# Kernel optimization log

Measured on AMD Instinct MI355X. Metric: run time of the kernel, lower is better.

The kernel has to match this reference:

```python
import jax, jax.numpy as jnp
import numpy as np

N_NODES = 100000
N_EDGES = 800000
F_IN, HID, N_CLS = 256, 128, 32


def setup_inputs() -> dict:
    key = jax.random.key(0)
    k1, k2, k3, k4, k5 = jax.random.split(key, 5)
    features = jax.random.normal(k1, (N_NODES, F_IN), dtype=jnp.float32)
    # random directed edges with no self loops (so add_remaining_self_loops == append all loops)
    src = jax.random.randint(k2, (N_EDGES,), 0, N_NODES)
    off = jax.random.randint(k3, (N_EDGES,), 1, N_NODES)
    dst = (src + off) % N_NODES
    edge_index = jnp.stack([src, dst]).astype(jnp.int64)
    # Glorot-style params for the two GCNConv layers
    W1 = jax.random.normal(k4, (F_IN, HID), dtype=jnp.float32) * (1.0 / np.sqrt(F_IN))
    b1 = jnp.zeros((HID,), dtype=jnp.float32)
    W2 = jax.random.normal(k5, (HID, N_CLS), dtype=jnp.float32) * (1.0 / np.sqrt(HID))
    b2 = jnp.zeros((N_CLS,), dtype=jnp.float32)
    return {"features": features, "edge_index": edge_index, "W1": W1, "b1": b1, "W2": W2, "b2": b2}


def _gcn_conv(x, W, b, src, dst, norm, n):
    xw = x @ W                                  # [N, d_out] dense GEMM
    msg = xw[src] * norm[:, None]               # gather + scale, [E, d_out]
    out = jax.ops.segment_sum(msg, dst, num_segments=n)  # scatter-add to targets
    return out + b


def reference(features, edge_index, W1, b1, W2, b2):
    n = features.shape[0]
    # add_remaining_self_loops (input has none, so append all)
    loops = jnp.arange(n, dtype=edge_index.dtype)
    src = jnp.concatenate([edge_index[0], loops])
    dst = jnp.concatenate([edge_index[1], loops])
    # gcn_norm: deg over targets, sym normalization deg^-1/2 A deg^-1/2
    deg = jax.ops.segment_sum(jnp.ones_like(src, dtype=features.dtype), dst, num_segments=n)
    dinv = jnp.where(deg > 0, jax.lax.rsqrt(deg), 0.0)
    norm = dinv[src] * dinv[dst]
    x = _gcn_conv(features, W1, b1, src, dst, norm, n)
    x = jax.nn.relu(x)
    # dropout is identity at inference (training=False)
    x = _gcn_conv(x, W2, b2, src, dst, norm, n)
    return jax.nn.log_softmax(x, axis=1)
```

## Files before the change

kernel.cpp:

```cpp
#include <hip/hip_runtime.h>
#include <hip/hip_bf16.h>

typedef __bf16 bf16_t;
typedef __attribute__((ext_vector_type(8))) __bf16 bf16x8;
typedef __attribute__((ext_vector_type(4))) float f32x4;

__global__ void k_deg_count(const int* __restrict__ dst, int* __restrict__ deg, int E) {
    int e = blockIdx.x * blockDim.x + threadIdx.x;
    if (e < E) atomicAdd(&deg[dst[e]], 1);
}

__global__ __launch_bounds__(256) void k_dinv_scan1(const int* __restrict__ deg,
                                                    float* __restrict__ dinv,
                                                    int* __restrict__ bsum, int n) {
    __shared__ int red[256];
    int b = blockIdx.x, t = threadIdx.x;
    int base = b * 1024 + t * 4;
    int s = 0;
#pragma unroll
    for (int j = 0; j < 4; ++j) {
        int i = base + j;
        if (i < n) { int d = deg[i]; s += d; dinv[i] = rsqrtf((float)(d + 1)); }
    }
    red[t] = s;
    __syncthreads();
    for (int d = 128; d > 0; d >>= 1) {
        if (t < d) red[t] += red[t + d];
        __syncthreads();
    }
    if (t == 0) bsum[b] = red[0];
}

__global__ __launch_bounds__(256) void k_scan2(int* __restrict__ bsum, int nb,
                                               int* __restrict__ rowPtr, int n) {
    __shared__ int s[256];
    int t = threadIdx.x;
    int v = (t < nb) ? bsum[t] : 0;
    s[t] = v;
    __syncthreads();
    for (int d = 1; d < 256; d <<= 1) {
        int u = (t >= d) ? s[t - d] : 0;
        __syncthreads();
        s[t] += u;
        __syncthreads();
    }
    if (t < nb) bsum[t] = s[t] - v;
    if (t == 255) rowPtr[n] = s[255];
}

__global__ __launch_bounds__(256) void k_scan3(const int* __restrict__ deg,
                                               const int* __restrict__ bsum,
                                               int* __restrict__ rowPtr, int n) {
    __shared__ int red[256];
    int b = blockIdx.x, t = threadIdx.x;
    int base = b * 1024 + t * 4;
    int v[4]; int s = 0;
#pragma unroll
    for (int j = 0; j < 4; ++j) { int i = base + j; v[j] = (i < n) ? deg[i] : 0; s += v[j]; }
    red[t] = s;
    __syncthreads();
    for (int d = 1; d < 256; d <<= 1) {
        int u = (t >= d) ? red[t - d] : 0;
        __syncthreads();
        red[t] += u;
        __syncthreads();
    }
    int run = bsum[b] + red[t] - s;
#pragma unroll
    for (int j = 0; j < 4; ++j) { int i = base + j; if (i < n) rowPtr[i] = run; run += v[j]; }
}

__global__ void k_scatter(const int* __restrict__ src, const int* __restrict__ dst,
                          const float* __restrict__ dinv, const int* __restrict__ rowPtr,
                          int* __restrict__ cursor, int2* __restrict__ edata, int E) {
    int e = blockIdx.x * blockDim.x + threadIdx.x;
    if (e >= E) return;
    int s = src[e], d = dst[e];
    int pos = rowPtr[d] + atomicAdd(&cursor[d], 1);
    int2 p; p.x = s; p.y = __float_as_int(dinv[s] * dinv[d]);
    edata[pos] = p;
}

__device__ inline void packB_one(const float* __restrict__ B, bf16_t* __restrict__ Bp,
                                 int N, int idx) {
    int j    = idx & 7;
    int lane = (idx >> 3) & 63;
    int st   = idx >> 9;
    int nt   = N >> 4;
    int s = st / nt, t = st - s * nt;
    int k = s * 32 + (lane >> 4) * 8 + j;
    int n = t * 16 + (lane & 15);
    Bp[idx] = (bf16_t)B[(size_t)k * N + n];
}

__global__ void k_packBoth(const float* __restrict__ W1, bf16_t* __restrict__ Bp1,
                           const float* __restrict__ W2, bf16_t* __restrict__ Bp2) {
    int idx = blockIdx.x * blockDim.x + threadIdx.x;
    const int T1 = (256 / 32) * (128 / 16) * 512;
    const int T2 = (128 / 32) * (32 / 16) * 512;
    if (idx < T1) packB_one(W1, Bp1, 128, idx);
    else if (idx < T1 + T2) packB_one(W2, Bp2, 32, idx - T1);
}

template <int KSTEPS, int NTILES>
__global__ __launch_bounds__(256) void k_gemm_pf32(
        const float* __restrict__ A, const bf16_t* __restrict__ Bp,
        bf16_t* __restrict__ C, int M) {
    int wave = (blockIdx.x * blockDim.x + threadIdx.x) >> 6;
    if (wave * 16 >= M) return;
    int lane = threadIdx.x & 63;
    int r16 = lane & 15, quad = lane >> 4;
    const int K = KSTEPS * 32, N = NTILES * 16;
    f32x4 acc[NTILES] = {};
    const float* arow = A + (size_t)(wave * 16 + r16) * K + quad * 8;
#pragma unroll
    for (int s = 0; s < KSTEPS; ++s) {
        const float* ap = arow + s * 32;
        bf16x8 a;
#pragma unroll
        for (int j = 0; j < 8; ++j) a[j] = (bf16_t)ap[j];
        const bf16_t* bp = Bp + ((size_t)(s * NTILES) * 64 + lane) * 8;
#pragma unroll
        for (int t = 0; t < NTILES; ++t) {
            bf16x8 b = *(const bf16x8*)(bp + t * 512);
            acc[t] = __builtin_amdgcn_mfma_f32_16x16x32_bf16(a, b, acc[t], 0, 0, 0);
        }
    }
#pragma unroll
    for (int t = 0; t < NTILES; ++t)
#pragma unroll
        for (int r = 0; r < 4; ++r)
            C[(size_t)(wave * 16 + quad * 4 + r) * N + t * 16 + r16] = (bf16_t)acc[t][r];
}

template <int KSTEPS, int NTILES>
__global__ __launch_bounds__(256) void k_gemm_pa16(
        const bf16_t* __restrict__ A, const bf16_t* __restrict__ Bp,
        bf16_t* __restrict__ C, int M) {
    int wave = (blockIdx.x * blockDim.x + threadIdx.x) >> 6;
    if (wave * 16 >= M) return;
    int lane = threadIdx.x & 63;
    int r16 = lane & 15, quad = lane >> 4;
    const int K = KSTEPS * 32, N = NTILES * 16;
    f32x4 acc[NTILES] = {};
    const bf16_t* arow = A + (size_t)(wave * 16 + r16) * K + quad * 8;
#pragma unroll
    for (int s = 0; s < KSTEPS; ++s) {
        bf16x8 a = *(const bf16x8*)(arow + s * 32);
        const bf16_t* bp = Bp + ((size_t)(s * NTILES) * 64 + lane) * 8;
#pragma unroll
        for (int t = 0; t < NTILES; ++t) {
            bf16x8 b = *(const bf16x8*)(bp + t * 512);
            acc[t] = __builtin_amdgcn_mfma_f32_16x16x32_bf16(a, b, acc[t], 0, 0, 0);
        }
    }
#pragma unroll
    for (int t = 0; t < NTILES; ++t)
#pragma unroll
        for (int r = 0; r < 4; ++r)
            C[(size_t)(wave * 16 + quad * 4 + r) * N + t * 16 + r16] = (bf16_t)acc[t][r];
}

__global__ __launch_bounds__(256) void k_agg1(
        const int* __restrict__ rowPtr, const int2* __restrict__ edata,
        const bf16_t* __restrict__ XW1, const float* __restrict__ dinv,
        const float* __restrict__ b1, bf16_t* __restrict__ H, int n) {
    int wave = (blockIdx.x * blockDim.x + threadIdx.x) >> 6;
    if (wave >= n) return;
    int lane = threadIdx.x & 63;
    int fl = (lane & 15) << 3;
    int h  = lane >> 4;
    int r0 = rowPtr[wave], r1 = rowPtr[wave + 1];
    float a0[8] = {}, a1[8] = {};
    int k = r0 + h;
    for (; k + 4 < r1; k += 8) {
        int2 e0 = edata[k], e1 = edata[k + 4];
        float w0 = __int_as_float(e0.y), w1 = __int_as_float(e1.y);
        bf16x8 x0 = *(const bf16x8*)(XW1 + ((size_t)e0.x << 7) + fl);
        bf16x8 x1 = *(const bf16x8*)(XW1 + ((size_t)e1.x << 7) + fl);
#pragma unroll
        for (int j = 0; j < 8; ++j) { a0[j] += (float)x0[j] * w0; a1[j] += (float)x1[j] * w1; }
    }
    if (k < r1) {
        int2 e0 = edata[k];
        float w0 = __int_as_float(e0.y);
        bf16x8 x0 = *(const bf16x8*)(XW1 + ((size_t)e0.x << 7) + fl);
#pragma unroll
        for (int j = 0; j < 8; ++j) a0[j] += (float)x0[j] * w0;
    }
#pragma unroll
    for (int j = 0; j < 8; ++j) {
        a0[j] += a1[j];
        a0[j] += __shfl_xor(a0[j], 16);
        a0[j] += __shfl_xor(a0[j], 32);
    }
    if (h == 0) {
        float d = dinv[wave], d2 = d * d;
        bf16x8 xs = *(const bf16x8*)(XW1 + ((size_t)wave << 7) + fl);
        bf16x8 hv;
#pragma unroll
        for (int j = 0; j < 8; ++j) {
            float v = a0[j] + (float)xs[j] * d2 + b1[fl + j];
            hv[j] = (bf16_t)fmaxf(v, 0.f);
        }
        *(bf16x8*)(H + ((size_t)wave << 7) + fl) = hv;
    }
}

__global__ __launch_bounds__(256) void k_agg2(
        const int* __restrict__ rowPtr, const int2* __restrict__ edata,
        const bf16_t* __restrict__ XW2, const float* __restrict__ dinv,
        const float* __restrict__ b2, float* __restrict__ out, int n) {
    int wave = (blockIdx.x * blockDim.x + threadIdx.x) >> 6;
    if (wave >= n) return;
    int lane = threadIdx.x & 63;
    int f = lane & 31, h = lane >> 5;
    int r0 = rowPtr[wave], r1 = rowPtr[wave + 1];
    float acc0 = 0.f, acc1 = 0.f;
    int k = r0 + h;
    for (; k + 2 < r1; k += 4) {
        int2 e0 = edata[k], e1 = edata[k + 2];
        acc0 += (float)XW2[((size_t)e0.x << 5) + f] * __int_as_float(e0.y);
        acc1 += (float)XW2[((size_t)e1.x << 5) + f] * __int_as_float(e1.y);
    }
    if (k < r1) {
        int2 e0 = edata[k];
        acc0 += (float)XW2[((size_t)e0.x << 5) + f] * __int_as_float(e0.y);
    }
    float acc = acc0 + acc1;
    acc += __shfl_xor(acc, 32);
    float d = dinv[wave];
    float v = acc + (float)XW2[((size_t)wave << 5) + f] * d * d + b2[f];
    float mx = v;
#pragma unroll
    for (int m = 16; m >= 1; m >>= 1) mx = fmaxf(mx, __shfl_xor(mx, m));
    float s = expf(v - mx);
#pragma unroll
    for (int m = 16; m >= 1; m >>= 1) s += __shfl_xor(s, m);
    if (lane < 32) out[((size_t)wave << 5) + f] = v - mx - logf(s);
}

extern "C" void kernel_launch(void* const* d_in, const int* in_sizes, int n_in,
                              void* d_out, int out_size, void* d_ws, size_t ws_size,
                              hipStream_t stream) {
    const float* feat = (const float*)d_in[0];
    const int*   eidx = (const int*)d_in[1];
    const float* W1   = (const float*)d_in[2];
    const float* b1   = (const float*)d_in[3];
    const float* W2   = (const float*)d_in[4];
    const float* b2   = (const float*)d_in[5];
    float* out = (float*)d_out;

    const int FIN = 256, HID = 128, NCLS = 32;
    const int N = in_sizes[0] / FIN;
    const int E = in_sizes[1] / 2;
    const int* src = eidx;
    const int* dst = eidx + E;

    char* ws = (char*)d_ws;
    size_t o = 0;
    auto alloc = [&](size_t bytes) -> void* {
        void* p = ws + o;
        o = (o + bytes + 255) & ~(size_t)255;
        return p;
    };
    int*    deg    = (int*)   alloc((size_t)N * 4);
    int*    cursor = (int*)   alloc((size_t)N * 4);
    size_t  zlen   = (size_t)((char*)(cursor + N) - (char*)deg);
    float*  dinv   = (float*) alloc((size_t)N * 4);
    int*    rowPtr = (int*)   alloc((size_t)(N + 1) * 4);
    int*    bsum   = (int*)   alloc(256 * 4);
    bf16_t* Bp1    = (bf16_t*)alloc((size_t)(FIN / 32) * (HID / 16) * 512 * 2);
    bf16_t* Bp2    = (bf16_t*)alloc((size_t)(HID / 32) * (NCLS / 16) * 512 * 2);
    int2*   edata  = (int2*)  alloc((size_t)E * 8);
    bf16_t* XW1    = (bf16_t*)alloc((size_t)N * HID * 2);
    bf16_t* H      = (bf16_t*)alloc((size_t)N * HID * 2);
    bf16_t* XW2    = XW1;

    const int T = 256;
    const int NB = (N + 1023) >> 10;
    hipMemsetAsync(deg, 0, zlen, stream);
    k_deg_count <<<(E + T - 1) / T, T, 0, stream>>>(dst, deg, E);
    k_dinv_scan1<<<NB, T, 0, stream>>>(deg, dinv, bsum, N);
    k_scan2     <<<1, T, 0, stream>>>(bsum, NB, rowPtr, N);
    k_scan3     <<<NB, T, 0, stream>>>(deg, bsum, rowPtr, N);
    k_scatter   <<<(E + T - 1) / T, T, 0, stream>>>(src, dst, dinv, rowPtr, cursor, edata, E);
    k_packBoth  <<<(32768 + 4096 + T - 1) / T, T, 0, stream>>>(W1, Bp1, W2, Bp2);

    {
        int waves = (N + 15) / 16;
        k_gemm_pf32<8, 8><<<(waves * 64 + T - 1) / T, T, 0, stream>>>(feat, Bp1, XW1, N);
    }
    k_agg1<<<(N * 64 + T - 1) / T, T, 0, stream>>>(rowPtr, edata, XW1, dinv, b1, H, N);

    {
        int waves = (N + 15) / 16;
        k_gemm_pa16<4, 2><<<(waves * 64 + T - 1) / T, T, 0, stream>>>(H, Bp2, XW2, N);
    }
    k_agg2<<<(N * 64 + T - 1) / T, T, 0, stream>>>(rowPtr, edata, XW2, dinv, b2, out, N);
}
```

Before: 370.3 us.

## Fuse layer-2 GEMM into aggregation, store source-only CSR, fold W1 pack into scan

The H @ W2 projection now happens inside the layer-1 aggregation kernel, using per-lane FP32 dot products and shuffle reductions. This removes the H buffer round trip and the separate bf16 GEMM launch. The CSR now stores only source indices and derives edge weights on the fly as dinv[src]*dinv[dst], which halves the edge payload but adds a dinv gather per edge. W1 packing is merged into scan3 and the W2 pack is dropped, saving two launches. The cost is extra FP32 math and W2 reads in every agg1 wave.

```diff
diff --git a/kernel.cpp b/kernel.cpp
--- a/kernel.cpp
+++ b/kernel.cpp
@@ -4,6 +4,7 @@
 typedef __bf16 bf16_t;
 typedef __attribute__((ext_vector_type(8))) __bf16 bf16x8;
 typedef __attribute__((ext_vector_type(4))) float f32x4;
+typedef __attribute__((ext_vector_type(8))) float f32x8;
 
 __global__ void k_deg_count(const int* __restrict__ dst, int* __restrict__ deg, int E) {
     int e = blockIdx.x * blockDim.x + threadIdx.x;
@@ -46,39 +47,6 @@
     }
     if (t < nb) bsum[t] = s[t] - v;
     if (t == 255) rowPtr[n] = s[255];
-}
-
-__global__ __launch_bounds__(256) void k_scan3(const int* __restrict__ deg,
-                                               const int* __restrict__ bsum,
-                                               int* __restrict__ rowPtr, int n) {
-    __shared__ int red[256];
-    int b = blockIdx.x, t = threadIdx.x;
-    int base = b * 1024 + t * 4;
-    int v[4]; int s = 0;
-#pragma unroll
-    for (int j = 0; j < 4; ++j) { int i = base + j; v[j] = (i < n) ? deg[i] : 0; s += v[j]; }
-    red[t] = s;
-    __syncthreads();
-    for (int d = 1; d < 256; d <<= 1) {
-        int u = (t >= d) ? red[t - d] : 0;
-        __syncthreads();
-        red[t] += u;
-        __syncthreads();
-    }
-    int run = bsum[b] + red[t] - s;
-#pragma unroll
-    for (int j = 0; j < 4; ++j) { int i = base + j; if (i < n) rowPtr[i] = run; run += v[j]; }
-}
-
-__global__ void k_scatter(const int* __restrict__ src, const int* __restrict__ dst,
-                          const float* __restrict__ dinv, const int* __restrict__ rowPtr,
-                          int* __restrict__ cursor, int2* __restrict__ edata, int E) {
-    int e = blockIdx.x * blockDim.x + threadIdx.x;
-    if (e >= E) return;
-    int s = src[e], d = dst[e];
-    int pos = rowPtr[d] + atomicAdd(&cursor[d], 1);
-    int2 p; p.x = s; p.y = __float_as_int(dinv[s] * dinv[d]);
-    edata[pos] = p;
 }
 
 __device__ inline void packB_one(const float* __restrict__ B, bf16_t* __restrict__ Bp,
@@ -93,13 +61,43 @@
     Bp[idx] = (bf16_t)B[(size_t)k * N + n];
 }
 
-__global__ void k_packBoth(const float* __restrict__ W1, bf16_t* __restrict__ Bp1,
-                           const float* __restrict__ W2, bf16_t* __restrict__ Bp2) {
-    int idx = blockIdx.x * blockDim.x + threadIdx.x;
+__global__ __launch_bounds__(256) void k_scan3(const int* __restrict__ deg,
+                                               const int* __restrict__ bsum,
+                                               int* __restrict__ rowPtr, int n,
+                                               const float* __restrict__ W1,
+                                               bf16_t* __restrict__ Bp1) {
+    __shared__ int red[256];
+    int b = blockIdx.x, t = threadIdx.x;
+    int base = b * 1024 + t * 4;
+    int v[4]; int s = 0;
+#pragma unroll
+    for (int j = 0; j < 4; ++j) { int i = base + j; v[j] = (i < n) ? deg[i] : 0; s += v[j]; }
+    red[t] = s;
+    __syncthreads();
+    for (int d = 1; d < 256; d <<= 1) {
+        int u = (t >= d) ? red[t - d] : 0;
+        __syncthreads();
+        red[t] += u;
+        __syncthreads();
+    }
+    int run = bsum[b] + red[t] - s;
+#pragma unroll
+    for (int j = 0; j < 4; ++j) { int i = base + j; if (i < n) rowPtr[i] = run; run += v[j]; }
+    int tid = b * 256 + t;
     const int T1 = (256 / 32) * (128 / 16) * 512;
-    const int T2 = (128 / 32) * (32 / 16) * 512;
-    if (idx < T1) packB_one(W1, Bp1, 128, idx);
-    else if (idx < T1 + T2) packB_one(W2, Bp2, 32, idx - T1);
+    if (tid < T1) packB_one(W1, Bp1, 128, tid);
+    int tid2 = tid + 25088;
+    if (tid2 < T1) packB_one(W1, Bp1, 128, tid2);
+}
+
+__global__ void k_scatter(const int* __restrict__ src, const int* __restrict__ dst,
+                          const int* __restrict__ rowPtr, int* __restrict__ cursor,
+                          int* __restrict__ esrc, int E) {
+    int e = blockIdx.x * blockDim.x + threadIdx.x;
+    if (e >= E) return;
+    int d = dst[e];
+    int pos = rowPtr[d] + atomicAdd(&cursor[d], 1);
+    esrc[pos] = src[e];
 }
 
 template <int KSTEPS, int NTILES>
@@ -133,38 +131,11 @@
             C[(size_t)(wave * 16 + quad * 4 + r) * N + t * 16 + r16] = (bf16_t)acc[t][r];
 }
 
-template <int KSTEPS, int NTILES>
-__global__ __launch_bounds__(256) void k_gemm_pa16(
-        const bf16_t* __restrict__ A, const bf16_t* __restrict__ Bp,
-        bf16_t* __restrict__ C, int M) {
-    int wave = (blockIdx.x * blockDim.x + threadIdx.x) >> 6;
-    if (wave * 16 >= M) return;
-    int lane = threadIdx.x & 63;
-    int r16 = lane & 15, quad = lane >> 4;
-    const int K = KSTEPS * 32, N = NTILES * 16;
-    f32x4 acc[NTILES] = {};
-    const bf16_t* arow = A + (size_t)(wave * 16 + r16) * K + quad * 8;
-#pragma unroll
-    for (int s = 0; s < KSTEPS; ++s) {
-        bf16x8 a = *(const bf16x8*)(arow + s * 32);
-        const bf16_t* bp = Bp + ((size_t)(s * NTILES) * 64 + lane) * 8;
-#pragma unroll
-        for (int t = 0; t < NTILES; ++t) {
-            bf16x8 b = *(const bf16x8*)(bp + t * 512);
-            acc[t] = __builtin_amdgcn_mfma_f32_16x16x32_bf16(a, b, acc[t], 0, 0, 0);
-        }
-    }
-#pragma unroll
-    for (int t = 0; t < NTILES; ++t)
-#pragma unroll
-        for (int r = 0; r < 4; ++r)
-            C[(size_t)(wave * 16 + quad * 4 + r) * N + t * 16 + r16] = (bf16_t)acc[t][r];
-}
-
 __global__ __launch_bounds__(256) void k_agg1(
-        const int* __restrict__ rowPtr, const int2* __restrict__ edata,
+        const int* __restrict__ rowPtr, const int* __restrict__ esrc,
         const bf16_t* __restrict__ XW1, const float* __restrict__ dinv,
-        const float* __restrict__ b1, bf16_t* __restrict__ H, int n) {
+        const float* __restrict__ b1, const float* __restrict__ W2,
+        bf16_t* __restrict__ XW2, int n) {
     int wave = (blockIdx.x * blockDim.x + threadIdx.x) >> 6;
     if (wave >= n) return;
     int lane = threadIdx.x & 63;
@@ -174,17 +145,17 @@
     float a0[8] = {}, a1[8] = {};
     int k = r0 + h;
     for (; k + 4 < r1; k += 8) {
-        int2 e0 = edata[k], e1 = edata[k + 4];
-        float w0 = __int_as_float(e0.y), w1 = __int_as_float(e1.y);
-        bf16x8 x0 = *(const bf16x8*)(XW1 + ((size_t)e0.x << 7) + fl);
-        bf16x8 x1 = *(const bf16x8*)(XW1 + ((size_t)e1.x << 7) + fl);
+        int s0 = esrc[k], s1 = esrc[k + 4];
+        float w0 = dinv[s0], w1 = dinv[s1];
+        bf16x8 x0 = *(const bf16x8*)(XW1 + ((size_t)s0 << 7) + fl);
+        bf16x8 x1 = *(const bf16x8*)(XW1 + ((size_t)s1 << 7) + fl);
 #pragma unroll
         for (int j = 0; j < 8; ++j) { a0[j] += (float)x0[j] * w0; a1[j] += (float)x1[j] * w1; }
     }
     if (k < r1) {
-        int2 e0 = edata[k];
-        float w0 = __int_as_float(e0.y);
-        bf16x8 x0 = *(const bf16x8*)(XW1 + ((size_t)e0.x << 7) + fl);
+        int s0 = esrc[k];
+        float w0 = dinv[s0];
+        bf16x8 x0 = *(const bf16x8*)(XW1 + ((size_t)s0 << 7) + fl);
 #pragma unroll
         for (int j = 0; j < 8; ++j) a0[j] += (float)x0[j] * w0;
     }
@@ -194,21 +165,38 @@
         a0[j] += __shfl_xor(a0[j], 16);
         a0[j] += __shfl_xor(a0[j], 32);
     }
-    if (h == 0) {
-        float d = dinv[wave], d2 = d * d;
-        bf16x8 xs = *(const bf16x8*)(XW1 + ((size_t)wave << 7) + fl);
-        bf16x8 hv;
-#pragma unroll
-        for (int j = 0; j < 8; ++j) {
-            float v = a0[j] + (float)xs[j] * d2 + b1[fl + j];
-            hv[j] = (bf16_t)fmaxf(v, 0.f);
-        }
-        *(bf16x8*)(H + ((size_t)wave << 7) + fl) = hv;
+    float d = dinv[wave];
+    bf16x8 xs = *(const bf16x8*)(XW1 + ((size_t)wave << 7) + fl);
+    float hrow[8];
+#pragma unroll
+    for (int j = 0; j < 8; ++j) {
+        float v = (a0[j] + (float)xs[j] * d) * d + b1[fl + j];
+        hrow[j] = fmaxf(v, 0.f);
+    }
+    float pc[8] = {};
+#pragma unroll
+    for (int j = 0; j < 8; ++j) {
+        f32x8 wr = *(const f32x8*)(W2 + (size_t)(fl + j) * 32 + h * 8);
+#pragma unroll
+        for (int c = 0; c < 8; ++c) pc[c] += hrow[j] * wr[c];
+    }
+#pragma unroll
+    for (int c = 0; c < 8; ++c) {
+        pc[c] += __shfl_xor(pc[c], 1);
+        pc[c] += __shfl_xor(pc[c], 2);
+        pc[c] += __shfl_xor(pc[c], 4);
+        pc[c] += __shfl_xor(pc[c], 8);
+    }
+    if ((lane & 15) == 0) {
+        bf16x8 pv;
+#pragma unroll
+        for (int c = 0; c < 8; ++c) pv[c] = (bf16_t)pc[c];
+        *(bf16x8*)(XW2 + ((size_t)wave << 5) + h * 8) = pv;
     }
 }
 
 __global__ __launch_bounds__(256) void k_agg2(
-        const int* __restrict__ rowPtr, const int2* __restrict__ edata,
+        const int* __restrict__ rowPtr, const int* __restrict__ esrc,
         const bf16_t* __restrict__ XW2, const float* __restrict__ dinv,
         const float* __restrict__ b2, float* __restrict__ out, int n) {
     int wave = (blockIdx.x * blockDim.x + threadIdx.x) >> 6;
@@ -219,18 +207,18 @@
     float acc0 = 0.f, acc1 = 0.f;
     int k = r0 + h;
     for (; k + 2 < r1; k += 4) {
-        int2 e0 = edata[k], e1 = edata[k + 2];
-        acc0 += (float)XW2[((size_t)e0.x << 5) + f] * __int_as_float(e0.y);
-        acc1 += (float)XW2[((size_t)e1.x << 5) + f] * __int_as_float(e1.y);
+        int s0 = esrc[k], s1 = esrc[k + 2];
+        acc0 += (float)XW2[((size_t)s0 << 5) + f] * dinv[s0];
+        acc1 += (float)XW2[((size_t)s1 << 5) + f] * dinv[s1];
     }
     if (k < r1) {
-        int2 e0 = edata[k];
-        acc0 += (float)XW2[((size_t)e0.x << 5) + f] * __int_as_float(e0.y);
+        int s0 = esrc[k];
+        acc0 += (float)XW2[((size_t)s0 << 5) + f] * dinv[s0];
     }
     float acc = acc0 + acc1;
     acc += __shfl_xor(acc, 32);
     float d = dinv[wave];
-    float v = acc + (float)XW2[((size_t)wave << 5) + f] * d * d + b2[f];
+    float v = (acc + (float)XW2[((size_t)wave << 5) + f] * d) * d + b2[f];
     float mx = v;
 #pragma unroll
     for (int m = 16; m >= 1; m >>= 1) mx = fmaxf(mx, __shfl_xor(mx, m));
@@ -271,11 +259,9 @@
     int*    rowPtr = (int*)   alloc((size_t)(N + 1) * 4);
     int*    bsum   = (int*)   alloc(256 * 4);
     bf16_t* Bp1    = (bf16_t*)alloc((size_t)(FIN / 32) * (HID / 16) * 512 * 2);
-    bf16_t* Bp2    = (bf16_t*)alloc((size_t)(HID / 32) * (NCLS / 16) * 512 * 2);
-    int2*   edata  = (int2*)  alloc((size_t)E * 8);
+    int*    esrc   = (int*)   alloc((size_t)E * 4);
     bf16_t* XW1    = (bf16_t*)alloc((size_t)N * HID * 2);
-    bf16_t* H      = (bf16_t*)alloc((size_t)N * HID * 2);
-    bf16_t* XW2    = XW1;
+    bf16_t* XW2    = (bf16_t*)alloc((size_t)N * NCLS * 2);
 
     const int T = 256;
     const int NB = (N + 1023) >> 10;
@@ -283,19 +269,13 @@
     k_deg_count <<<(E + T - 1) / T, T, 0, stream>>>(dst, deg, E);
     k_dinv_scan1<<<NB, T, 0, stream>>>(deg, dinv, bsum, N);
     k_scan2     <<<1, T, 0, stream>>>(bsum, NB, rowPtr, N);
-    k_scan3     <<<NB, T, 0, stream>>>(deg, bsum, rowPtr, N);
-    k_scatter   <<<(E + T - 1) / T, T, 0, stream>>>(src, dst, dinv, rowPtr, cursor, edata, E);
-    k_packBoth  <<<(32768 + 4096 + T - 1) / T, T, 0, stream>>>(W1, Bp1, W2, Bp2);
+    k_scan3     <<<NB, T, 0, stream>>>(deg, bsum, rowPtr, N, W1, Bp1);
+    k_scatter   <<<(E + T - 1) / T, T, 0, stream>>>(src, dst, rowPtr, cursor, esrc, E);
 
     {
         int waves = (N + 15) / 16;
         k_gemm_pf32<8, 8><<<(waves * 64 + T - 1) / T, T, 0, stream>>>(feat, Bp1, XW1, N);
     }
-    k_agg1<<<(N * 64 + T - 1) / T, T, 0, stream>>>(rowPtr, edata, XW1, dinv, b1, H, N);
-
-    {
-        int waves = (N + 15) / 16;
-        k_gemm_pa16<4, 2><<<(waves * 64 + T - 1) / T, T, 0, stream>>>(H, Bp2, XW2, N);
-    }
-    k_agg2<<<(N * 64 + T - 1) / T, T, 0, stream>>>(rowPtr, edata, XW2, dinv, b2, out, N);
-}
+    k_agg1<<<(N * 64 + T - 1) / T, T, 0, stream>>>(rowPtr, esrc, XW1, dinv, b1, W2, XW2, N);
+    k_agg2<<<(N * 64 + T - 1) / T, T, 0, stream>>>(rowPtr, esrc, XW2, dinv, b2, out, N);
+}
```

Result: slower. 511.3 us (+38.1%).

## Fuse graph preprocessing into one persistent kernel with grid barriers

Applied to the files above, without the earlier changes.

Replaces the memset plus six preprocessing kernels (degree count, three-stage scan, scatter, weight pack) with one persistent 256-block kernel that uses atomic grid barriers between phases. The aim is to remove per-kernel launch gaps and the extra memset. In exchange, the degree atomics and scatter run with only 256 blocks and grid-stride loops, which may lower parallelism. Correctness also depends on all 256 blocks being co-resident, and the fixed CHUNK of 392 assumes N is at most 256*392.

```diff
diff --git a/kernel.cpp b/kernel.cpp
--- a/kernel.cpp
+++ b/kernel.cpp
@@ -5,80 +5,20 @@
 typedef __attribute__((ext_vector_type(8))) __bf16 bf16x8;
 typedef __attribute__((ext_vector_type(4))) float f32x4;
 
-__global__ void k_deg_count(const int* __restrict__ dst, int* __restrict__ deg, int E) {
-    int e = blockIdx.x * blockDim.x + threadIdx.x;
-    if (e < E) atomicAdd(&deg[dst[e]], 1);
-}
-
-__global__ __launch_bounds__(256) void k_dinv_scan1(const int* __restrict__ deg,
-                                                    float* __restrict__ dinv,
-                                                    int* __restrict__ bsum, int n) {
-    __shared__ int red[256];
-    int b = blockIdx.x, t = threadIdx.x;
-    int base = b * 1024 + t * 4;
-    int s = 0;
-#pragma unroll
-    for (int j = 0; j < 4; ++j) {
-        int i = base + j;
-        if (i < n) { int d = deg[i]; s += d; dinv[i] = rsqrtf((float)(d + 1)); }
-    }
-    red[t] = s;
-    __syncthreads();
-    for (int d = 128; d > 0; d >>= 1) {
-        if (t < d) red[t] += red[t + d];
-        __syncthreads();
-    }
-    if (t == 0) bsum[b] = red[0];
-}
-
-__global__ __launch_bounds__(256) void k_scan2(int* __restrict__ bsum, int nb,
-                                               int* __restrict__ rowPtr, int n) {
-    __shared__ int s[256];
-    int t = threadIdx.x;
-    int v = (t < nb) ? bsum[t] : 0;
-    s[t] = v;
-    __syncthreads();
-    for (int d = 1; d < 256; d <<= 1) {
-        int u = (t >= d) ? s[t - d] : 0;
-        __syncthreads();
-        s[t] += u;
-        __syncthreads();
-    }
-    if (t < nb) bsum[t] = s[t] - v;
-    if (t == 255) rowPtr[n] = s[255];
-}
-
-__global__ __launch_bounds__(256) void k_scan3(const int* __restrict__ deg,
-                                               const int* __restrict__ bsum,
-                                               int* __restrict__ rowPtr, int n) {
-    __shared__ int red[256];
-    int b = blockIdx.x, t = threadIdx.x;
-    int base = b * 1024 + t * 4;
-    int v[4]; int s = 0;
-#pragma unroll
-    for (int j = 0; j < 4; ++j) { int i = base + j; v[j] = (i < n) ? deg[i] : 0; s += v[j]; }
-    red[t] = s;
-    __syncthreads();
-    for (int d = 1; d < 256; d <<= 1) {
-        int u = (t >= d) ? red[t - d] : 0;
-        __syncthreads();
-        red[t] += u;
-        __syncthreads();
-    }
-    int run = bsum[b] + red[t] - s;
-#pragma unroll
-    for (int j = 0; j < 4; ++j) { int i = base + j; if (i < n) rowPtr[i] = run; run += v[j]; }
-}
-
-__global__ void k_scatter(const int* __restrict__ src, const int* __restrict__ dst,
-                          const float* __restrict__ dinv, const int* __restrict__ rowPtr,
-                          int* __restrict__ cursor, int2* __restrict__ edata, int E) {
-    int e = blockIdx.x * blockDim.x + threadIdx.x;
-    if (e >= E) return;
-    int s = src[e], d = dst[e];
-    int pos = rowPtr[d] + atomicAdd(&cursor[d], 1);
-    int2 p; p.x = s; p.y = __float_as_int(dinv[s] * dinv[d]);
-    edata[pos] = p;
+#define NBLK 256
+#define THR  256
+#define CHUNK 392
+
+__device__ inline void grid_barrier(int* bar, int idx) {
+    __syncthreads();
+    __threadfence();
+    if (threadIdx.x == 0) {
+        __hip_atomic_fetch_add(&bar[idx], 1, __ATOMIC_RELEASE, __HIP_MEMORY_SCOPE_AGENT);
+        while (__hip_atomic_load(&bar[idx], __ATOMIC_ACQUIRE, __HIP_MEMORY_SCOPE_AGENT) < NBLK)
+            __builtin_amdgcn_s_sleep(2);
+    }
+    __syncthreads();
+    __threadfence();
 }
 
 __device__ inline void packB_one(const float* __restrict__ B, bf16_t* __restrict__ Bp,
@@ -93,13 +33,65 @@
     Bp[idx] = (bf16_t)B[(size_t)k * N + n];
 }
 
-__global__ void k_packBoth(const float* __restrict__ W1, bf16_t* __restrict__ Bp1,
-                           const float* __restrict__ W2, bf16_t* __restrict__ Bp2) {
-    int idx = blockIdx.x * blockDim.x + threadIdx.x;
-    const int T1 = (256 / 32) * (128 / 16) * 512;
-    const int T2 = (128 / 32) * (32 / 16) * 512;
-    if (idx < T1) packB_one(W1, Bp1, 128, idx);
-    else if (idx < T1 + T2) packB_one(W2, Bp2, 32, idx - T1);
+__global__ __launch_bounds__(THR) void k_prep(
+        const int* __restrict__ src, const int* __restrict__ dst, int E, int n,
+        int* __restrict__ deg, int* __restrict__ cursor, float* __restrict__ dinv,
+        int* __restrict__ rowPtr, int* __restrict__ bsum, int* __restrict__ bar,
+        const float* __restrict__ W1, bf16_t* __restrict__ Bp1,
+        const float* __restrict__ W2, bf16_t* __restrict__ Bp2,
+        int2* __restrict__ edata) {
+    int b = blockIdx.x, t = threadIdx.x;
+    int tid = b * THR + t;
+    const int nthr = NBLK * THR;
+    for (int i = tid; i < n; i += nthr) { deg[i] = 0; cursor[i] = 0; }
+    if (tid < 32768) packB_one(W1, Bp1, 128, tid);
+    else if (tid < 32768 + 4096) packB_one(W2, Bp2, 32, tid - 32768);
+    grid_barrier(bar, 0);
+    for (int e = tid; e < E; e += nthr) atomicAdd(&deg[dst[e]], 1);
+    grid_barrier(bar, 1);
+    __shared__ int red[THR];
+    __shared__ int sb[NBLK];
+    int base = b * CHUNK + 2 * t;
+    int d0 = 0, d1 = 0;
+    if (2 * t < CHUNK) {
+        if (base < n)     { d0 = deg[base];     dinv[base]     = rsqrtf((float)(d0 + 1)); }
+        if (base + 1 < n) { d1 = deg[base + 1]; dinv[base + 1] = rsqrtf((float)(d1 + 1)); }
+    }
+    int pair = d0 + d1;
+    red[t] = pair;
+    __syncthreads();
+    for (int dd = 1; dd < THR; dd <<= 1) {
+        int u = (t >= dd) ? red[t - dd] : 0;
+        __syncthreads();
+        red[t] += u;
+        __syncthreads();
+    }
+    int excl_t = red[t] - pair;
+    if (t == THR - 1) bsum[b] = red[THR - 1];
+    grid_barrier(bar, 2);
+    int bv = bsum[t];
+    sb[t] = bv;
+    __syncthreads();
+    for (int dd = 1; dd < NBLK; dd <<= 1) {
+        int u = (t >= dd) ? sb[t - dd] : 0;
+        __syncthreads();
+        sb[t] += u;
+        __syncthreads();
+    }
+    if (b == 0 && t == 0) rowPtr[n] = sb[NBLK - 1];
+    int excl_b = (b == 0) ? 0 : sb[b - 1];
+    int run = excl_b + excl_t;
+    if (2 * t < CHUNK) {
+        if (base < n)     rowPtr[base]     = run;
+        if (base + 1 < n) rowPtr[base + 1] = run + d0;
+    }
+    grid_barrier(bar, 3);
+    for (int e = tid; e < E; e += nthr) {
+        int s = src[e], d = dst[e];
+        int pos = rowPtr[d] + atomicAdd(&cursor[d], 1);
+        int2 p; p.x = s; p.y = __float_as_int(dinv[s] * dinv[d]);
+        edata[pos] = p;
+    }
 }
 
 template <int KSTEPS, int NTILES>
@@ -122,8 +114,8 @@
         const bf16_t* bp = Bp + ((size_t)(s * NTILES) * 64 + lane) * 8;
 #pragma unroll
         for (int t = 0; t < NTILES; ++t) {
-            bf16x8 b = *(const bf16x8*)(bp + t * 512);
-            acc[t] = __builtin_amdgcn_mfma_f32_16x16x32_bf16(a, b, acc[t], 0, 0, 0);
+            bf16x8 bfrag = *(const bf16x8*)(bp + t * 512);
+            acc[t] = __builtin_amdgcn_mfma_f32_16x16x32_bf16(a, bfrag, acc[t], 0, 0, 0);
         }
     }
 #pragma unroll
@@ -150,8 +142,8 @@
         const bf16_t* bp = Bp + ((size_t)(s * NTILES) * 64 + lane) * 8;
 #pragma unroll
         for (int t = 0; t < NTILES; ++t) {
-            bf16x8 b = *(const bf16x8*)(bp + t * 512);
-            acc[t] = __builtin_amdgcn_mfma_f32_16x16x32_bf16(a, b, acc[t], 0, 0, 0);
+            bf16x8 bfrag = *(const bf16x8*)(bp + t * 512);
+            acc[t] = __builtin_amdgcn_mfma_f32_16x16x32_bf16(a, bfrag, acc[t], 0, 0, 0);
         }
     }
 #pragma unroll
@@ -266,10 +258,10 @@
     };
     int*    deg    = (int*)   alloc((size_t)N * 4);
     int*    cursor = (int*)   alloc((size_t)N * 4);
-    size_t  zlen   = (size_t)((char*)(cursor + N) - (char*)deg);
     float*  dinv   = (float*) alloc((size_t)N * 4);
     int*    rowPtr = (int*)   alloc((size_t)(N + 1) * 4);
-    int*    bsum   = (int*)   alloc(256 * 4);
+    int*    bsum   = (int*)   alloc(NBLK * 4);
+    int*    bar    = (int*)   alloc(256);
     bf16_t* Bp1    = (bf16_t*)alloc((size_t)(FIN / 32) * (HID / 16) * 512 * 2);
     bf16_t* Bp2    = (bf16_t*)alloc((size_t)(HID / 32) * (NCLS / 16) * 512 * 2);
     int2*   edata  = (int2*)  alloc((size_t)E * 8);
@@ -278,14 +270,9 @@
     bf16_t* XW2    = XW1;
 
     const int T = 256;
-    const int NB = (N + 1023) >> 10;
-    hipMemsetAsync(deg, 0, zlen, stream);
-    k_deg_count <<<(E + T - 1) / T, T, 0, stream>>>(dst, deg, E);
-    k_dinv_scan1<<<NB, T, 0, stream>>>(deg, dinv, bsum, N);
-    k_scan2     <<<1, T, 0, stream>>>(bsum, NB, rowPtr, N);
-    k_scan3     <<<NB, T, 0, stream>>>(deg, bsum, rowPtr, N);
-    k_scatter   <<<(E + T - 1) / T, T, 0, stream>>>(src, dst, dinv, rowPtr, cursor, edata, E);
-    k_packBoth  <<<(32768 + 4096 + T - 1) / T, T, 0, stream>>>(W1, Bp1, W2, Bp2);
+    hipMemsetAsync(bar, 0, 16, stream);
+    k_prep<<<NBLK, THR, 0, stream>>>(src, dst, E, N, deg, cursor, dinv,
+                                     rowPtr, bsum, bar, W1, Bp1, W2, Bp2, edata);
 
     {
         int waves = (N + 15) / 16;
```

After: 554.8 us. +49.8%, slower.
